# Performance work log

Hardware: AMD Instinct MI355X
Metric: run time of the kernel (lower is better)

## Reference

```python
import jax, jax.numpy as jnp
import numpy as np

K_BINS = 8192
HIDDEN = 2048
SQRT2 = 1.4142135623730951
LEAKY_SLOPE = 0.01
TMIN = 1e-10


def setup_inputs() -> dict:
    key = jax.random.key(0)
    k0, k1, k2 = jax.random.split(key, 3)
    D = 2 * K_BINS  # mu length so that cat([mu, t]) has 2K+1 features
    # positive mu keeps mu ** (gamma - 1/(1-gamma)) (a fractional power) finite
    mu = jax.random.uniform(k0, (D,), jnp.float32, 0.1, 1.0)
    t = jnp.array([0.5], jnp.float32)
    gamma = jnp.array([0.5], jnp.float32)  # 1/(1-gamma) = 2 -> integral exponent
    W1 = jax.random.normal(k1, (D + 1, HIDDEN), jnp.float32) * (1.0 / np.sqrt(D + 1))
    b1 = jnp.zeros((HIDDEN,), jnp.float32)
    W2 = jax.random.normal(k2, (HIDDEN, D), jnp.float32) * (1.0 / np.sqrt(HIDDEN))
    b2 = jnp.zeros((D,), jnp.float32)
    return {"mu": mu, "t": t, "gamma": gamma, "W1": W1, "b1": b1,
            "W2": W2, "b2": b2, "K": K_BINS}


def reference(mu, t, gamma, W1, b1, W2, b2, K):
    g = gamma[0]
    # --- NN(cat([mu, t])) -> (mu_epsilon, ln_sigma_epsilon), each [K] ---
    inp = jnp.concatenate([mu, t])                      # [2K+1]
    h = jax.nn.leaky_relu(inp @ W1 + b1, LEAKY_SLOPE)   # [hidden]
    out = h @ W2 + b2                                   # [2K]
    mu_eps, ln_sig = out[:K], out[K:]
    # --- mu_x / sigma_x (t < tmin branch folded in via where) ---
    p_mu = g - 1.0 / (1.0 - g)
    p_eps = 1.0 / (1.0 - g)
    mu_x_nn = jnp.power(mu[:K], p_mu) * jnp.power(mu_eps, p_eps)
    sigma_x_nn = jnp.power(1.0 - g, -0.5) * jnp.exp(0.5 * ln_sig)
    use_nn = t[0] >= TMIN
    mu_x = jnp.where(use_nn, mu_x_nn, jnp.zeros_like(mu_eps))     # [K]
    sigma_x = jnp.where(use_nn, sigma_x_nn, jnp.ones_like(mu_eps))  # [K]
    # --- vectorized discretised CDF differences over the (D_out, K) grid ---
    kk = jnp.arange(K, dtype=jnp.float32)
    kl = 2.0 * (kk - 1.0) / (K - 1.0)   # left bin edges  [K]
    kr = 2.0 * kk / (K - 1.0)           # right bin edges [K]

    def cdf(x):  # x: [K] edges -> G: [D_out, K]
        z = (x[None, :] - mu_x[:, None]) / (sigma_x[:, None] * SQRT2)
        F = 0.5 * (1.0 + jax.lax.erf(z))
        return jnp.where(x[None, :] <= -1.0, 0.0,
                         jnp.where(x[None, :] >= 1.0, 1.0, F))

    return cdf(kr) - cdf(kl)  # [K, K] per-bin probabilities
```

## Files before the change

### kernel.cpp

```cpp
#include <hip/hip_runtime.h>
#include <math.h>

#define KBINS 8192
#define DDIM  16384
#define HID   2048
#define LASTROW 16384

#define C1 16
#define NB1 1024
#define C2 8
#define NB2 256

static constexpr float SQRT2_F  = 1.4142135623730951f;
static constexpr float INVSQ2PI = 0.3989422804014327f;

__device__ __forceinline__ float fast_erff(float x) {
    float ax = fabsf(x);
    float t  = 1.0f / fmaf(0.3275911f, ax, 1.0f);
    float p  = t * (0.254829592f +
               t * (-0.284496736f +
               t * (1.421413741f +
               t * (-1.453152027f +
               t * 1.061405429f))));
    float r = 1.0f - p * __expf(-ax * ax);
    return copysignf(r, x);
}

__global__ void __launch_bounds__(256)
mv1_partial(const float* __restrict__ mu, const float* __restrict__ W1,
            float* __restrict__ part1) {
    __shared__ float a_s[C1];
    int r0 = blockIdx.x * C1;
    if (threadIdx.x < C1) a_s[threadIdx.x] = mu[r0 + threadIdx.x];
    __syncthreads();
    int c0 = threadIdx.x * 4;
    float4 acc0 = {0.f, 0.f, 0.f, 0.f};
    float4 acc1 = {0.f, 0.f, 0.f, 0.f};
    const float* wp = W1 + (size_t)r0 * HID;
#pragma unroll
    for (int k = 0; k < C1; ++k) {
        float a = a_s[k];
        const float4 w0 = *reinterpret_cast<const float4*>(wp + (size_t)k * HID + c0);
        const float4 w1 = *reinterpret_cast<const float4*>(wp + (size_t)k * HID + c0 + 1024);
        acc0.x += a * w0.x; acc0.y += a * w0.y; acc0.z += a * w0.z; acc0.w += a * w0.w;
        acc1.x += a * w1.x; acc1.y += a * w1.y; acc1.z += a * w1.z; acc1.w += a * w1.w;
    }
    float* pp = part1 + (size_t)blockIdx.x * HID;
    *reinterpret_cast<float4*>(pp + c0)        = acc0;
    *reinterpret_cast<float4*>(pp + c0 + 1024) = acc1;
}

__global__ void __launch_bounds__(256)
mv2h(const float* __restrict__ part1, const float* __restrict__ b1,
     const float* __restrict__ W1, const float* __restrict__ t,
     const float* __restrict__ W2, float* __restrict__ part2) {
    __shared__ float red[32][8];
    __shared__ float hs[C2];
    int r0    = blockIdx.y * C2;
    int cbase = blockIdx.x * 8192;
    int col_l = threadIdx.x & 7;
    int sub   = threadIdx.x >> 3;
    {
        float s = 0.f;
        const float* p = part1 + r0 + col_l;
#pragma unroll 8
        for (int m = 0; m < 32; ++m)
            s += p[(size_t)(sub + (m << 5)) * HID];
        red[sub][col_l] = s;
    }
    __syncthreads();
    if (threadIdx.x < C2) {
        int r = r0 + threadIdx.x;
        float v = b1[r] + t[0] * W1[(size_t)LASTROW * HID + r];
#pragma unroll
        for (int p = 0; p < 32; ++p) v += red[p][threadIdx.x];
        hs[threadIdx.x] = (v >= 0.f) ? v : 0.01f * v;
    }
    __syncthreads();
    int c0 = threadIdx.x * 4;
    float4 acc[8];
#pragma unroll
    for (int q = 0; q < 8; ++q) acc[q] = {0.f, 0.f, 0.f, 0.f};
    const float* wp = W2 + (size_t)r0 * DDIM + cbase + c0;
#pragma unroll 2
    for (int k = 0; k < C2; ++k) {
        float a = hs[k];
        const float* wr = wp + (size_t)k * DDIM;
#pragma unroll
        for (int q = 0; q < 8; ++q) {
            const float4 w = *reinterpret_cast<const float4*>(wr + q * 1024);
            acc[q].x += a * w.x; acc[q].y += a * w.y;
            acc[q].z += a * w.z; acc[q].w += a * w.w;
        }
    }
    float* pp = part2 + (size_t)blockIdx.y * DDIM + cbase + c0;
#pragma unroll
    for (int q = 0; q < 8; ++q)
        *reinterpret_cast<float4*>(pp + q * 1024) = acc[q];
}

__global__ void __launch_bounds__(256)
scalars(const float* __restrict__ part2, const float* __restrict__ b2,
        const float* __restrict__ mu, const float* __restrict__ t,
        const float* __restrict__ gamma,
        float* __restrict__ mu_x, float* __restrict__ sigma_x) {
    __shared__ float red0[8][32];
    __shared__ float red1[8][32];
    int col_l = threadIdx.x & 31;
    int sub   = threadIdx.x >> 5;
    int c     = blockIdx.x * 32 + col_l;
    float s0 = 0.f, s1 = 0.f;
    const float* p0 = part2 + c;
    const float* p1 = part2 + c + KBINS;
#pragma unroll 8
    for (int m = 0; m < 32; ++m) {
        size_t off = (size_t)(sub + (m << 3)) * DDIM;
        s0 += p0[off];
        s1 += p1[off];
    }
    red0[sub][col_l] = s0;
    red1[sub][col_l] = s1;
    __syncthreads();
    if (threadIdx.x < 32) {
        int cc = blockIdx.x * 32 + threadIdx.x;
        float v0 = b2[cc];
        float v1 = b2[cc + KBINS];
#pragma unroll
        for (int p = 0; p < 8; ++p) { v0 += red0[p][threadIdx.x]; v1 += red1[p][threadIdx.x]; }
        float g  = gamma[0];
        float pe = 1.0f / (1.0f - g);
        float pm = g - pe;
        bool use_nn = (t[0] >= 1e-10f);
        float mx = powf(mu[cc], pm) * powf(v0, pe);
        float sx = powf(1.0f - g, -0.5f) * expf(0.5f * v1);
        mu_x[cc]    = use_nn ? mx : 0.0f;
        sigma_x[cc] = use_nn ? sx : 1.0f;
    }
}

__global__ void __launch_bounds__(256)
cdf_row(const float* __restrict__ mu_x, const float* __restrict__ sigma_x,
        float* __restrict__ out) {
    int tid = threadIdx.x;
    for (int rr = 0; rr < 2; ++rr) {
        int i = blockIdx.x * 2 + rr;
        float m    = mu_x[i];
        float invs = 1.0f / sigma_x[i];
        const float sc = 2.0f / 8191.0f;
        float A    = sc * invs;
        float B    = (-1.0f / 8191.0f - m) * invs;
        float coef = INVSQ2PI * A;
        float* orow = out + (size_t)i * KBINS;
#pragma unroll
        for (int it = 0; it < 8; ++it) {
            int j0 = it * 1024 + tid * 4;
            float4 r;
            if (j0 < 4096) {
                float u0 = fmaf((float)j0, A, B);
                float u1 = u0 + A;
                float u2 = u1 + A;
                float u3 = u2 + A;
                r.x = coef * __expf(-0.5f * u0 * u0);
                r.y = coef * __expf(-0.5f * u1 * u1);
                r.z = coef * __expf(-0.5f * u2 * u2);
                r.w = coef * __expf(-0.5f * u3 * u3);
            } else if (j0 == 4096) {
                float z = (8190.0f / 8191.0f - m) * invs * (1.0f / SQRT2_F);
                r.x = 0.5f * (1.0f - fast_erff(z));
                r.y = r.z = r.w = 0.f;
            } else {
                r.x = r.y = r.z = r.w = 0.f;
            }
            *reinterpret_cast<float4*>(orow + j0) = r;
        }
    }
}

extern "C" void kernel_launch(void* const* d_in, const int* in_sizes, int n_in,
                              void* d_out, int out_size, void* d_ws, size_t ws_size,
                              hipStream_t stream) {
    const float* mu    = (const float*)d_in[0];
    const float* t     = (const float*)d_in[1];
    const float* gamma = (const float*)d_in[2];
    const float* W1    = (const float*)d_in[3];
    const float* b1    = (const float*)d_in[4];
    const float* W2    = (const float*)d_in[5];
    const float* b2    = (const float*)d_in[6];
    float* out = (float*)d_out;

    float* ws      = (float*)d_ws;
    float* part1   = ws;
    float* part2   = part1 + (size_t)NB1 * HID;
    float* mu_x    = part2 + (size_t)NB2 * DDIM;
    float* sigma_x = mu_x + KBINS;

    mv1_partial<<<dim3(NB1),     dim3(256), 0, stream>>>(mu, W1, part1);
    mv2h       <<<dim3(2, NB2),  dim3(256), 0, stream>>>(part1, b1, W1, t, W2, part2);
    scalars    <<<dim3(256),     dim3(256), 0, stream>>>(part2, b2, mu, t, gamma, mu_x, sigma_x);
    cdf_row    <<<dim3(4096),    dim3(256), 0, stream>>>(mu_x, sigma_x, out);
}
```

Before: 144.2 us.

## Fuse all stages into one cooperative persistent kernel with grid syncs

Replaces the four separate launches with a single cooperative kernel that runs the W1 matvec, the hidden reduction, the W2 matvec, and the per-row scalar computation plus CDF output writes as grid-stride phases separated by grid.sync(). Per-row mu_x/sigma_x are computed in shared memory just before each 8-row block of output is written, and h is reduced once into a global buffer. The aim is to remove inter-kernel launch gaps and the round trip of mu_x and sigma_x through global memory. In exchange it depends on cooperative launch support, caps the grid at resident-block occupancy (at most 1024 blocks), and pays for grid-wide barriers. It falls back to the old four-kernel path if the cooperative launch fails.

```diff
diff --git a/kernel.cpp b/kernel.cpp
--- a/kernel.cpp
+++ b/kernel.cpp
@@ -1,15 +1,16 @@
 #include <hip/hip_runtime.h>
+#include <hip/hip_cooperative_groups.h>
 #include <math.h>
+
+namespace cg = cooperative_groups;
 
 #define KBINS 8192
 #define DDIM  16384
 #define HID   2048
 #define LASTROW 16384
 
-#define C1 16
-#define NB1 1024
-#define C2 8
-#define NB2 256
+#define NCH1 1024
+#define NCH2 256
 
 static constexpr float SQRT2_F  = 1.4142135623730951f;
 static constexpr float INVSQ2PI = 0.3989422804014327f;
@@ -27,18 +28,184 @@
 }
 
 __global__ void __launch_bounds__(256)
+fused(const float* __restrict__ mu, const float* __restrict__ t,
+      const float* __restrict__ gamma, const float* __restrict__ W1,
+      const float* __restrict__ b1, const float* __restrict__ W2,
+      const float* __restrict__ b2, float* __restrict__ out,
+      float* __restrict__ part1, float* __restrict__ h,
+      float* __restrict__ part2) {
+    cg::grid_group grid = cg::this_grid();
+    const int tid = threadIdx.x;
+    const int G   = gridDim.x;
+
+    __shared__ float a_s[16];
+    __shared__ float red[16][17];
+    __shared__ float hs8[8];
+    __shared__ float s01[2][8];
+    __shared__ float sA[8], sB[8], sCf[8], sEr[8];
+
+    for (int ch = blockIdx.x; ch < NCH1; ch += G) {
+        int r0 = ch * 16;
+        if (tid < 16) a_s[tid] = mu[r0 + tid];
+        __syncthreads();
+        int c0 = tid * 4;
+        float4 acc0 = {0.f, 0.f, 0.f, 0.f};
+        float4 acc1 = {0.f, 0.f, 0.f, 0.f};
+        const float* wp = W1 + (size_t)r0 * HID;
+#pragma unroll
+        for (int k = 0; k < 16; ++k) {
+            float a = a_s[k];
+            const float4 w0 = *reinterpret_cast<const float4*>(wp + (size_t)k * HID + c0);
+            const float4 w1 = *reinterpret_cast<const float4*>(wp + (size_t)k * HID + c0 + 1024);
+            acc0.x += a * w0.x; acc0.y += a * w0.y; acc0.z += a * w0.z; acc0.w += a * w0.w;
+            acc1.x += a * w1.x; acc1.y += a * w1.y; acc1.z += a * w1.z; acc1.w += a * w1.w;
+        }
+        float* pp = part1 + (size_t)ch * HID;
+        *reinterpret_cast<float4*>(pp + c0)        = acc0;
+        *reinterpret_cast<float4*>(pp + c0 + 1024) = acc1;
+        __syncthreads();
+    }
+    grid.sync();
+
+    for (int cb = blockIdx.x; cb < 128; cb += G) {
+        int c0    = cb * 16;
+        int col_l = tid & 15;
+        int sub   = tid >> 4;
+        float s = 0.f;
+        const float* p = part1 + c0 + col_l;
+#pragma unroll 8
+        for (int m = 0; m < 64; ++m)
+            s += p[(size_t)(sub + (m << 4)) * HID];
+        red[sub][col_l] = s;
+        __syncthreads();
+        if (tid < 16) {
+            int c = c0 + tid;
+            float v = b1[c] + t[0] * W1[(size_t)LASTROW * HID + c];
+#pragma unroll
+            for (int q = 0; q < 16; ++q) v += red[q][tid];
+            h[c] = (v >= 0.f) ? v : 0.01f * v;
+        }
+        __syncthreads();
+    }
+    grid.sync();
+
+    for (int cq = blockIdx.x; cq < NCH1; cq += G) {
+        int ch    = cq >> 2;
+        int quar  = cq & 3;
+        int r0    = ch * 8;
+        int cbase = quar * 4096;
+        if (tid < 8) hs8[tid] = h[r0 + tid];
+        __syncthreads();
+        float4 acc[4];
+#pragma unroll
+        for (int q = 0; q < 4; ++q) acc[q] = {0.f, 0.f, 0.f, 0.f};
+        const float* wp = W2 + (size_t)r0 * DDIM + cbase + tid * 4;
+#pragma unroll
+        for (int k = 0; k < 8; ++k) {
+            float a = hs8[k];
+            const float* wr = wp + (size_t)k * DDIM;
+#pragma unroll
+            for (int q = 0; q < 4; ++q) {
+                const float4 w = *reinterpret_cast<const float4*>(wr + q * 1024);
+                acc[q].x += a * w.x; acc[q].y += a * w.y;
+                acc[q].z += a * w.z; acc[q].w += a * w.w;
+            }
+        }
+        float* pp = part2 + (size_t)ch * DDIM + cbase + tid * 4;
+#pragma unroll
+        for (int q = 0; q < 4; ++q)
+            *reinterpret_cast<float4*>(pp + q * 1024) = acc[q];
+        __syncthreads();
+    }
+    grid.sync();
+
+    for (int rb = blockIdx.x; rb < 1024; rb += G) {
+        int r0 = rb * 8;
+        {
+            int col_l = tid & 7;
+            int half  = (tid >> 3) & 1;
+            int sub   = tid >> 4;
+            int c     = r0 + col_l + half * KBINS;
+            float s = 0.f;
+            const float* p = part2 + c;
+#pragma unroll 8
+            for (int m = 0; m < 16; ++m)
+                s += p[(size_t)(sub + (m << 4)) * DDIM];
+            red[sub][half * 8 + col_l] = s;
+            __syncthreads();
+            if (tid < 16) {
+                int hlf = tid >> 3, cl = tid & 7;
+                float v = b2[r0 + cl + hlf * KBINS];
+#pragma unroll
+                for (int q = 0; q < 16; ++q) v += red[q][tid];
+                s01[hlf][cl] = v;
+            }
+            __syncthreads();
+            if (tid < 8) {
+                float s0 = s01[0][tid];
+                float s1 = s01[1][tid];
+                float g  = gamma[0];
+                float pe = 1.0f / (1.0f - g);
+                float pm = g - pe;
+                bool use_nn = (t[0] >= 1e-10f);
+                float mval = use_nn ? powf(mu[r0 + tid], pm) * powf(s0, pe) : 0.0f;
+                float invs = use_nn ? powf(1.0f - g, 0.5f) * expf(-0.5f * s1) : 1.0f;
+                const float sc = 2.0f / 8191.0f;
+                float A    = sc * invs;
+                sA[tid]  = A;
+                sB[tid]  = (-1.0f / 8191.0f - mval) * invs;
+                sCf[tid] = INVSQ2PI * A;
+                float z = (8190.0f / 8191.0f - mval) * invs * (1.0f / SQRT2_F);
+                sEr[tid] = 0.5f * (1.0f - fast_erff(z));
+            }
+            __syncthreads();
+        }
+#pragma unroll 2
+        for (int rr = 0; rr < 8; ++rr) {
+            int i = r0 + rr;
+            float A    = sA[rr];
+            float B    = sB[rr];
+            float coef = sCf[rr];
+            float* orow = out + (size_t)i * KBINS;
+#pragma unroll
+            for (int it = 0; it < 8; ++it) {
+                int j0 = it * 1024 + tid * 4;
+                float4 r;
+                if (j0 < 4096) {
+                    float u0 = fmaf((float)j0, A, B);
+                    float u1 = u0 + A;
+                    float u2 = u1 + A;
+                    float u3 = u2 + A;
+                    r.x = coef * __expf(-0.5f * u0 * u0);
+                    r.y = coef * __expf(-0.5f * u1 * u1);
+                    r.z = coef * __expf(-0.5f * u2 * u2);
+                    r.w = coef * __expf(-0.5f * u3 * u3);
+                } else if (j0 == 4096) {
+                    r.x = sEr[rr];
+                    r.y = r.z = r.w = 0.f;
+                } else {
+                    r.x = r.y = r.z = r.w = 0.f;
+                }
+                *reinterpret_cast<float4*>(orow + j0) = r;
+            }
+        }
+        __syncthreads();
+    }
+}
+
+__global__ void __launch_bounds__(256)
 mv1_partial(const float* __restrict__ mu, const float* __restrict__ W1,
             float* __restrict__ part1) {
-    __shared__ float a_s[C1];
-    int r0 = blockIdx.x * C1;
-    if (threadIdx.x < C1) a_s[threadIdx.x] = mu[r0 + threadIdx.x];
+    __shared__ float a_s[16];
+    int r0 = blockIdx.x * 16;
+    if (threadIdx.x < 16) a_s[threadIdx.x] = mu[r0 + threadIdx.x];
     __syncthreads();
     int c0 = threadIdx.x * 4;
     float4 acc0 = {0.f, 0.f, 0.f, 0.f};
     float4 acc1 = {0.f, 0.f, 0.f, 0.f};
     const float* wp = W1 + (size_t)r0 * HID;
 #pragma unroll
-    for (int k = 0; k < C1; ++k) {
+    for (int k = 0; k < 16; ++k) {
         float a = a_s[k];
         const float4 w0 = *reinterpret_cast<const float4*>(wp + (size_t)k * HID + c0);
         const float4 w1 = *reinterpret_cast<const float4*>(wp + (size_t)k * HID + c0 + 1024);
@@ -55,8 +222,8 @@
      const float* __restrict__ W1, const float* __restrict__ t,
      const float* __restrict__ W2, float* __restrict__ part2) {
     __shared__ float red[32][8];
-    __shared__ float hs[C2];
-    int r0    = blockIdx.y * C2;
+    __shared__ float hs[8];
+    int r0    = blockIdx.y * 8;
     int cbase = blockIdx.x * 8192;
     int col_l = threadIdx.x & 7;
     int sub   = threadIdx.x >> 3;
@@ -69,7 +236,7 @@
         red[sub][col_l] = s;
     }
     __syncthreads();
-    if (threadIdx.x < C2) {
+    if (threadIdx.x < 8) {
         int r = r0 + threadIdx.x;
         float v = b1[r] + t[0] * W1[(size_t)LASTROW * HID + r];
 #pragma unroll
@@ -83,7 +250,7 @@
     for (int q = 0; q < 8; ++q) acc[q] = {0.f, 0.f, 0.f, 0.f};
     const float* wp = W2 + (size_t)r0 * DDIM + cbase + c0;
 #pragma unroll 2
-    for (int k = 0; k < C2; ++k) {
+    for (int k = 0; k < 8; ++k) {
         float a = hs[k];
         const float* wr = wp + (size_t)k * DDIM;
 #pragma unroll
@@ -188,14 +355,34 @@
     const float* b2    = (const float*)d_in[6];
     float* out = (float*)d_out;
 
-    float* ws      = (float*)d_ws;
-    float* part1   = ws;
-    float* part2   = part1 + (size_t)NB1 * HID;
-    float* mu_x    = part2 + (size_t)NB2 * DDIM;
-    float* sigma_x = mu_x + KBINS;
-
-    mv1_partial<<<dim3(NB1),     dim3(256), 0, stream>>>(mu, W1, part1);
-    mv2h       <<<dim3(2, NB2),  dim3(256), 0, stream>>>(part1, b1, W1, t, W2, part2);
-    scalars    <<<dim3(256),     dim3(256), 0, stream>>>(part2, b2, mu, t, gamma, mu_x, sigma_x);
-    cdf_row    <<<dim3(4096),    dim3(256), 0, stream>>>(mu_x, sigma_x, out);
-}
+    float* ws    = (float*)d_ws;
+    float* part1 = ws;
+    float* h     = part1 + (size_t)NCH1 * HID;
+    float* part2 = h + HID;
+    float* mu_x  = part2 + (size_t)NCH2 * DDIM;
+    float* sig_x = mu_x + KBINS;
+
+    int dev = 0;
+    (void)hipGetDevice(&dev);
+    int coop = 0, ncu = 0, nb = 0;
+    (void)hipDeviceGetAttribute(&coop, hipDeviceAttributeCooperativeLaunch, dev);
+    (void)hipDeviceGetAttribute(&ncu, hipDeviceAttributeMultiprocessorCount, dev);
+    (void)hipOccupancyMaxActiveBlocksPerMultiprocessor(&nb, (const void*)fused, 256, 0);
+
+    hipError_t err = hipErrorUnknown;
+    long maxg = (long)nb * (long)ncu;
+    int G = (int)((maxg > 1024) ? 1024 : maxg);
+    if (coop && G >= 256) {
+        void* args[] = {(void*)&mu, (void*)&t, (void*)&gamma, (void*)&W1, (void*)&b1,
+                        (void*)&W2, (void*)&b2, (void*)&out, (void*)&part1, (void*)&h,
+                        (void*)&part2};
+        err = hipLaunchCooperativeKernel((const void*)fused, dim3(G), dim3(256), args, 0, stream);
+    }
+    if (err != hipSuccess) {
+        (void)hipGetLastError();
+        mv1_partial<<<dim3(NCH1),     dim3(256), 0, stream>>>(mu, W1, part1);
+        mv2h       <<<dim3(2, NCH2),  dim3(256), 0, stream>>>(part1, b1, W1, t, W2, part2);
+        scalars    <<<dim3(256),      dim3(256), 0, stream>>>(part2, b2, mu, t, gamma, mu_x, sig_x);
+        cdf_row    <<<dim3(4096),     dim3(256), 0, stream>>>(mu_x, sig_x, out);
+    }
+}
```

Result: slower. 386.4 us (+168.0%).
